# Kernel optimization log

Measured on AMD Instinct MI355X. Metric: run time of the kernel, lower is better.

The kernel has to match this reference:

```python
import jax, jax.numpy as jnp
import numpy as np

D = 256      # d_model
A = 64       # attn_dim
K = 16       # k_neighbors
N = 20000    # embedding table rows
B = 32768    # batch of perturbed genes
SCALE = A ** -0.5
EPS = 1e-5


def setup_inputs() -> dict:
    key = jax.random.key(0)
    ks = jax.random.split(key, 12)
    all_embs = jax.random.normal(ks[0], (N, D), dtype=jnp.float32)
    center_idx = jax.random.randint(ks[1], (B,), 0, N)
    nb_idx = jax.random.randint(ks[2], (B, K), 0, N)
    nb_weights = jax.random.uniform(ks[3], (B, K), dtype=jnp.float32)
    # learned params (torch Linear weight layout: [out, in])
    s = lambda fan_in: 1.0 / np.sqrt(fan_in)
    Wq = jax.random.uniform(ks[4], (A, D), minval=-s(D), maxval=s(D))
    Wk = jax.random.uniform(ks[5], (A, D), minval=-s(D), maxval=s(D))
    Wg = jax.random.uniform(ks[6], (D, D), minval=-s(D), maxval=s(D))
    bg = jax.random.uniform(ks[7], (D,), minval=-s(D), maxval=s(D))
    Wo = jax.random.uniform(ks[8], (D, 2 * D), minval=-s(2 * D), maxval=s(2 * D))
    bo = jax.random.uniform(ks[9], (D,), minval=-s(2 * D), maxval=s(2 * D))
    gamma = jnp.ones((D,), jnp.float32)
    beta = jnp.zeros((D,), jnp.float32)
    return dict(all_embs=all_embs, center_idx=center_idx, nb_idx=nb_idx,
                nb_weights=nb_weights, Wq=Wq, Wk=Wk, Wg=Wg, bg=bg,
                Wo=Wo, bo=bo, gamma=gamma, beta=beta)


def reference(all_embs, center_idx, nb_idx, nb_weights, Wq, Wk, Wg, bg, Wo, bo, gamma, beta):
    center = all_embs[center_idx]                      # [B, D]
    nbs = all_embs[nb_idx]                             # [B, K, D]
    q = center @ Wq.T                                  # [B, A]
    k = jnp.einsum('bkd,ad->bka', nbs, Wk)             # [B, K, A]
    logits = jnp.einsum('ba,bka->bk', q, k) * SCALE
    logits = logits + jnp.log(jnp.clip(nb_weights, 1e-6))
    attn = jax.nn.softmax(logits, axis=-1)             # [B, K]
    gate = jax.nn.sigmoid(center @ Wg.T + bg)          # [B, D]
    context = gate * jnp.einsum('bk,bkd->bd', attn, nbs)
    combined = jnp.concatenate([center, context], axis=-1)  # [B, 2D]
    enriched = combined @ Wo.T + bo                    # [B, D]
    x = enriched + center
    mu = jnp.mean(x, axis=-1, keepdims=True)
    var = jnp.var(x, axis=-1, keepdims=True)
    return (x - mu) * jax.lax.rsqrt(var + EPS) * gamma + beta
```

## Files before the change

kernel.cpp:

```cpp
#include <hip/hip_runtime.h>

#define DD 256
#define MM 16

typedef __attribute__((ext_vector_type(8))) short bfrag;
typedef __attribute__((ext_vector_type(4))) float ffrag;

__device__ __forceinline__ float lo2f(unsigned int p){ union{unsigned int i; float f;} v; v.i = p<<16; return v.f; }
__device__ __forceinline__ float hi2f(unsigned int p){ union{unsigned int i; float f;} v; v.i = p & 0xffff0000u; return v.f; }
__device__ __forceinline__ float bf2f(unsigned short u){ union{unsigned int i; float f;} v; v.i = ((unsigned int)u)<<16; return v.f; }
__device__ __forceinline__ unsigned short f2b(float x){
    union{float f; unsigned int i;} v; v.f = x;
    unsigned int r = v.i + 0x7fffu + ((v.i>>16)&1u);
    return (unsigned short)(r>>16);
}
__device__ __forceinline__ unsigned int pack2(float a, float b){
    return (unsigned int)f2b(a) | ((unsigned int)f2b(b)<<16);
}

__device__ __forceinline__ int swz256(int d, int e){
    return ((d>>4)*8 + (e>>5))*512 + (((e>>3)&3)*16 + (d&15))*8 + (e&7);
}
__device__ __forceinline__ int swz512(int d, int e){
    return ((d>>4)*16 + (e>>5))*512 + (((e>>3)&3)*16 + (d&15))*8 + (e&7);
}

extern "C" __global__ __launch_bounds__(256)
void prep_all(const float* __restrict__ Wq, const float* __restrict__ Wk,
              const float* __restrict__ Wg, const float* __restrict__ Wo,
              const float* __restrict__ embs, unsigned short* __restrict__ ws, int n8)
{
    int bid = blockIdx.x, e = threadIdx.x;
    if (bid < 256) {
        int d = bid; float acc = 0.f;
        #pragma unroll 8
        for (int a = 0; a < 64; ++a) acc = fmaf(Wq[a*256 + e], Wk[a*256 + d], acc);
        ws[swz256(d, e)] = f2b(acc);
    } else if (bid < 512) {
        int r = bid - 256;
        ws[65536 + swz256(r, e)] = f2b(Wg[r*256 + e]);
    } else if (bid < 768) {
        int r = bid - 512;
        ws[131072 + swz512(r, e)]       = f2b(Wo[r*512 + e]);
        ws[131072 + swz512(r, e + 256)] = f2b(Wo[r*512 + 256 + e]);
    } else {
        int i = (bid - 768)*256 + e;
        if (i < n8) {
            const float4* s = (const float4*)embs + (size_t)i*2;
            float4 a = s[0], b = s[1];
            uint4 o;
            o.x = pack2(a.x,a.y); o.y = pack2(a.z,a.w);
            o.z = pack2(b.x,b.y); o.w = pack2(b.z,b.w);
            ((uint4*)(ws + 262144))[i] = o;
        }
    }
}

template<bool TBF>
__device__ __forceinline__ void gather8(uint4* buf, const unsigned short* tbl,
                                        const float* embs, int idx, int p)
{
    if (TBF) {
        const unsigned short* base = tbl + (size_t)idx*DD + p*8;
        #pragma unroll
        for (int i = 0; i < 8; ++i) buf[i] = *(const uint4*)(base + i*32);
    } else {
        const float* base = embs + (size_t)idx*DD + p*8;
        #pragma unroll
        for (int i = 0; i < 8; ++i) {
            float4 a = *(const float4*)(base + i*32);
            float4 b = *(const float4*)(base + i*32 + 4);
            buf[i].x = pack2(a.x,a.y); buf[i].y = pack2(a.z,a.w);
            buf[i].z = pack2(b.x,b.y); buf[i].w = pack2(b.z,b.w);
        }
    }
}

template<bool TBF>
__global__ __launch_bounds__(256, 3)
void na_mfma6(const float* __restrict__ embs,
              const int* __restrict__ cidx,
              const int* __restrict__ nidx,
              const float* __restrict__ nbw,
              const unsigned short* __restrict__ tbl,
              const unsigned short* __restrict__ wMt,
              const unsigned short* __restrict__ wWg,
              const unsigned short* __restrict__ wWo,
              const float* __restrict__ bg,
              const float* __restrict__ bo,
              const float* __restrict__ gamma,
              const float* __restrict__ beta,
              float* __restrict__ out)
{
    __shared__ __align__(16) unsigned short s_ax[16][264];
    __shared__ __align__(16) unsigned short s_t[16][264];
    __shared__ __align__(16) unsigned short s_nb[4][16][264];
    __shared__ float s_attn[4][16];
    __shared__ int   s_cidx[16];
    float* s_x = (float*)&s_nb[0][0][0];

    const int tid  = threadIdx.x;
    const int row0 = blockIdx.x * MM;
    const int lane = tid & 63, wv = tid >> 6;
    const int l15  = lane & 15, quad = lane >> 4;
    const ffrag fz = {0.f, 0.f, 0.f, 0.f};

    if (tid < 16) s_cidx[tid] = cidx[row0 + tid];
    uint4 careg[8];
    {
        int aidx = cidx[row0 + l15];
        if (TBF) {
            const unsigned short* p = tbl + (size_t)aidx*DD + quad*8;
            #pragma unroll
            for (int kc = 0; kc < 8; ++kc) careg[kc] = *(const uint4*)(p + kc*32);
        } else {
            const float* p = embs + (size_t)aidx*DD + quad*8;
            #pragma unroll
            for (int kc = 0; kc < 8; ++kc) {
                float4 a = *(const float4*)(p + kc*32);
                float4 b = *(const float4*)(p + kc*32 + 4);
                careg[kc].x = pack2(a.x,a.y); careg[kc].y = pack2(a.z,a.w);
                careg[kc].z = pack2(b.x,b.y); careg[kc].w = pack2(b.z,b.w);
            }
        }
    }

    {
        ffrag at[4] = {fz,fz,fz,fz}, ag[4] = {fz,fz,fz,fz};
        const unsigned short* btA = wMt + (size_t)(wv*4)*4096 + lane*8;
        const unsigned short* bgA = wWg + (size_t)(wv*4)*4096 + lane*8;
        #pragma unroll
        for (int kc = 0; kc < 8; ++kc) {
            bfrag af = *(const bfrag*)&careg[kc];
            #pragma unroll
            for (int t = 0; t < 4; ++t) {
                at[t] = __builtin_amdgcn_mfma_f32_16x16x32_bf16(af, *(const bfrag*)(btA + t*4096 + kc*512), at[t], 0,0,0);
                ag[t] = __builtin_amdgcn_mfma_f32_16x16x32_bf16(af, *(const bfrag*)(bgA + t*4096 + kc*512), ag[t], 0,0,0);
            }
        }
        #pragma unroll
        for (int t = 0; t < 4; ++t) {
            int col = wv*64 + t*16 + l15;
            float bgv = bg[col];
            #pragma unroll
            for (int r = 0; r < 4; ++r) {
                int rr = quad*4 + r;
                s_t[rr][col]  = f2b(at[t][r]);
                float g = 1.f / (1.f + expf(-(ag[t][r] + bgv)));
                s_ax[rr][col] = f2b(g);
            }
        }
    }
    __syncthreads();

    {
        const int k = lane >> 2;
        const int p = lane & 3;
        int idxs[4];
        #pragma unroll
        for (int j = 0; j < 4; ++j)
            idxs[j] = nidx[(size_t)(row0 + 4*wv + j) * 16 + k];

        uint4 buf[2][8];
        gather8<TBF>(buf[0], tbl, embs, idxs[0], p);

        #pragma unroll
        for (int j = 0; j < 4; ++j) {
            if (j < 3) gather8<TBF>(buf[(j+1)&1], tbl, embs, idxs[j+1], p);
            const int m = 4*wv + j;
            unsigned short* nbp = &s_nb[wv][k][p*8];
            #pragma unroll
            for (int i = 0; i < 8; ++i) *(uint4*)(nbp + i*32) = buf[j&1][i];
            const unsigned short* trow = &s_t[m][p*8];
            float part = 0.f;
            #pragma unroll
            for (int i = 0; i < 8; ++i) {
                uint4 v = buf[j&1][i];
                uint4 tv = *(const uint4*)(trow + i*32);
                part += lo2f(v.x)*lo2f(tv.x) + hi2f(v.x)*hi2f(tv.x)
                      + lo2f(v.y)*lo2f(tv.y) + hi2f(v.y)*hi2f(tv.y)
                      + lo2f(v.z)*lo2f(tv.z) + hi2f(v.z)*hi2f(tv.z)
                      + lo2f(v.w)*lo2f(tv.w) + hi2f(v.w)*hi2f(tv.w);
            }
            part += __shfl_xor(part, 1);
            part += __shfl_xor(part, 2);
            float lg = part * 0.125f;
            float mx = lg;
            mx = fmaxf(mx, __shfl_xor(mx, 4));  mx = fmaxf(mx, __shfl_xor(mx, 8));
            mx = fmaxf(mx, __shfl_xor(mx, 16)); mx = fmaxf(mx, __shfl_xor(mx, 32));
            float wgt = fmaxf(nbw[(size_t)(row0 + m) * 16 + k], 1e-6f);
            float e = wgt * __expf(lg - mx);
            float s = e;
            s += __shfl_xor(s, 4);  s += __shfl_xor(s, 8);
            s += __shfl_xor(s, 16); s += __shfl_xor(s, 32);
            float attn = e / s;
            if (p == 0) s_attn[wv][k] = attn;
            float4 aw0 = *(const float4*)&s_attn[wv][0];
            float4 aw1 = *(const float4*)&s_attn[wv][4];
            float4 aw2 = *(const float4*)&s_attn[wv][8];
            float4 aw3 = *(const float4*)&s_attn[wv][12];
            float aarr[16] = {aw0.x,aw0.y,aw0.z,aw0.w, aw1.x,aw1.y,aw1.z,aw1.w,
                              aw2.x,aw2.y,aw2.z,aw2.w, aw3.x,aw3.y,aw3.z,aw3.w};
            float c0=0.f, c1=0.f, c2=0.f, c3=0.f;
            #pragma unroll
            for (int kk = 0; kk < 16; ++kk) {
                uint2 v = *(const uint2*)&s_nb[wv][kk][lane*4];
                float a = aarr[kk];
                c0 += a * lo2f(v.x); c1 += a * hi2f(v.x);
                c2 += a * lo2f(v.y); c3 += a * hi2f(v.y);
            }
            uint2 g = *(const uint2*)&s_ax[m][lane*4];
            c0 *= lo2f(g.x); c1 *= hi2f(g.x); c2 *= lo2f(g.y); c3 *= hi2f(g.y);
            uint2 o; o.x = pack2(c0, c1); o.y = pack2(c2, c3);
            *(uint2*)&s_ax[m][lane*4] = o;
        }
    }
    __syncthreads();

    {
        ffrag acc[4] = {fz,fz,fz,fz};
        const unsigned short* arx = &s_ax[l15][quad * 8];
        const unsigned short* bO  = wWo + (size_t)(wv*4)*8192 + lane*8;
        #pragma unroll
        for (int kc = 0; kc < 8; ++kc) {
            bfrag af = *(const bfrag*)&careg[kc];
            #pragma unroll
            for (int t = 0; t < 4; ++t)
                acc[t] = __builtin_amdgcn_mfma_f32_16x16x32_bf16(af, *(const bfrag*)(bO + t*8192 + kc*512), acc[t], 0,0,0);
        }
        #pragma unroll
        for (int kc = 8; kc < 16; ++kc) {
            bfrag af = *(const bfrag*)(arx + (kc-8)*32);
            #pragma unroll
            for (int t = 0; t < 4; ++t)
                acc[t] = __builtin_amdgcn_mfma_f32_16x16x32_bf16(af, *(const bfrag*)(bO + t*8192 + kc*512), acc[t], 0,0,0);
        }
        #pragma unroll
        for (int t = 0; t < 4; ++t) {
            int col = wv*64 + t*16 + l15;
            float bov = bo[col];
            #pragma unroll
            for (int r = 0; r < 4; ++r) {
                int rr = quad*4 + r;
                float ctr = embs[(size_t)s_cidx[rr] * DD + col];
                s_x[rr*260 + col] = acc[t][r] + bov + ctr;
            }
        }
    }
    __syncthreads();

    {
        #pragma unroll
        for (int jj = 0; jj < 4; ++jj) {
            int m = wv * 4 + jj;
            const float* xr = s_x + m*260;
            float x0 = xr[lane],       x1 = xr[64 + lane];
            float x2 = xr[128 + lane], x3 = xr[192 + lane];
            float s  = x0 + x1 + x2 + x3;
            float ss = x0*x0 + x1*x1 + x2*x2 + x3*x3;
            #pragma unroll
            for (int off = 32; off >= 1; off >>= 1) {
                s  += __shfl_xor(s, off);
                ss += __shfl_xor(ss, off);
            }
            float mu  = s * (1.f/256.f);
            float var = ss * (1.f/256.f) - mu*mu;
            float rs  = rsqrtf(var + 1e-5f);
            size_t base = (size_t)(row0 + m) * DD;
            float xs[4] = {x0, x1, x2, x3};
            #pragma unroll
            for (int cc = 0; cc < 4; ++cc) {
                int dd = cc*64 + lane;
                out[base + dd] = (xs[cc] - mu) * rs * gamma[dd] + beta[dd];
            }
        }
    }
}

#define SD 260
#define KT 16
#define WS 17
extern "C" __global__ __launch_bounds__(256)
void na_f32_kernel(const float* __restrict__ embs, const int* __restrict__ center_idx,
                   const int* __restrict__ nb_idx, const float* __restrict__ nb_w,
                   const float* __restrict__ Wq, const float* __restrict__ Wk,
                   const float* __restrict__ Wg, const float* __restrict__ bg,
                   const float* __restrict__ Wo, const float* __restrict__ bo,
                   const float* __restrict__ gamma, const float* __restrict__ beta,
                   float* __restrict__ out)
{
    __shared__ __align__(16) float s_center[MM][SD];
    __shared__ __align__(16) float s_tc[MM][SD];
    __shared__ __align__(16) float s_nb[16][SD];
    __shared__ __align__(16) float s_w[DD][WS];
    __shared__ __align__(16) float s_q[MM][64];
    __shared__ float s_red[16][16];
    __shared__ float s_attn[16];
    const int tid = threadIdx.x;
    const int row0 = blockIdx.x * MM;
    const int td = tid & 63, tm = tid >> 6;
    {
        int m = tid >> 4, c = tid & 15;
        int idx = center_idx[row0 + m];
        const float4* src = (const float4*)(embs + (size_t)idx * DD) + c * 4;
        float4* dst = (float4*)&s_center[m][c * 16];
        dst[0]=src[0]; dst[1]=src[1]; dst[2]=src[2]; dst[3]=src[3];
    }
    __syncthreads();
    {
        const int a = tid & 63, mg = tid >> 6;
        float qacc[4] = {0,0,0,0};
        for (int kt = 0; kt < DD; kt += KT) {
            __syncthreads();
            { int r = tid >> 2, c4 = (tid & 3) * 4;
              *(float4*)&s_w[r][c4] = *(const float4*)(Wq + r * DD + kt + c4); }
            __syncthreads();
            #pragma unroll
            for (int kk = 0; kk < KT; kk += 4) {
                float4 b = *(const float4*)&s_w[a][kk];
                #pragma unroll
                for (int i = 0; i < 4; ++i) {
                    float4 av = *(const float4*)&s_center[4*mg + i][kt + kk];
                    qacc[i] += av.x*b.x + av.y*b.y + av.z*b.z + av.w*b.w;
                }
            }
        }
        __syncthreads();
        #pragma unroll
        for (int i = 0; i < 4; ++i) s_q[4*mg + i][a] = qacc[i];
    }
    __syncthreads();
    {
        float tacc[4][4];
        #pragma unroll
        for (int i=0;i<4;++i) { tacc[i][0]=tacc[i][1]=tacc[i][2]=tacc[i][3]=0.f; }
        for (int kk = 0; kk < 64; kk += 4) {
            float4 bk[4];
            #pragma unroll
            for (int t4 = 0; t4 < 4; ++t4)
                bk[t4] = *(const float4*)(Wk + (size_t)(kk + t4) * DD + 4 * td);
            #pragma unroll
            for (int i = 0; i < 4; ++i) {
                float4 av = *(const float4*)&s_q[4*tm + i][kk];
                tacc[i][0] += av.x*bk[0].x + av.y*bk[1].x + av.z*bk[2].x + av.w*bk[3].x;
                tacc[i][1] += av.x*bk[0].y + av.y*bk[1].y + av.z*bk[2].y + av.w*bk[3].y;
                tacc[i][2] += av.x*bk[0].z + av.y*bk[1].z + av.z*bk[2].z + av.w*bk[3].z;
                tacc[i][3] += av.x*bk[0].w + av.y*bk[1].w + av.z*bk[2].w + av.w*bk[3].w;
            }
        }
        #pragma unroll
        for (int i = 0; i < 4; ++i)
            *(float4*)&s_tc[4*tm + i][4*td] = make_float4(tacc[i][0],tacc[i][1],tacc[i][2],tacc[i][3]);
    }
    __syncthreads();
    for (int m = 0; m < MM; ++m) {
        { int k = tid >> 4, c = tid & 15;
          int idx = nb_idx[(row0 + m) * 16 + k];
          const float4* src = (const float4*)(embs + (size_t)idx * DD) + c * 4;
          float4* dst = (float4*)&s_nb[k][c * 16];
          dst[0]=src[0]; dst[1]=src[1]; dst[2]=src[2]; dst[3]=src[3]; }
        __syncthreads();
        { int k = tid >> 4, i = tid & 15;
          float acc = 0.f;
          #pragma unroll
          for (int j4 = 0; j4 < 4; ++j4) {
              float4 nv = *(const float4*)&s_nb[k][i*16 + 4*j4];
              float4 tv = *(const float4*)&s_tc[m][i*16 + 4*j4];
              acc += nv.x*tv.x + nv.y*tv.y + nv.z*tv.z + nv.w*tv.w;
          }
          s_red[k][i] = acc; }
        __syncthreads();
        if (tid < 16) {
            float lg = 0.f;
            #pragma unroll
            for (int i = 0; i < 16; ++i) lg += s_red[tid][i];
            float wv2 = nb_w[(row0 + m) * 16 + tid];
            lg = lg * 0.125f + logf(fmaxf(wv2, 1e-6f));
            float mx = lg;
            #pragma unroll
            for (int off = 8; off >= 1; off >>= 1) mx = fmaxf(mx, __shfl_xor(mx, off));
            float e = expf(lg - mx);
            float s = e;
            #pragma unroll
            for (int off = 8; off >= 1; off >>= 1) s += __shfl_xor(s, off);
            s_attn[tid] = e / s;
        }
        __syncthreads();
        { float acc = 0.f;
// ... 93 lines not shown
            float mu = s * (1.f/256.f);
            float var = ss * (1.f/256.f) - mu*mu;
            float rs = rsqrtf(var + 1e-5f);
            size_t base = (size_t)(row0 + m) * DD;
            float xs[4] = {x0,x1,x2,x3};
            #pragma unroll
            for (int c = 0; c < 4; ++c) {
                int dd = c*64 + lane;
                out[base + dd] = (xs[c] - mu) * rs * gamma[dd] + beta[dd];
            }
        }
    }
}

extern "C" void kernel_launch(void* const* d_in, const int* in_sizes, int n_in,
                              void* d_out, int out_size, void* d_ws, size_t ws_size,
                              hipStream_t stream) {
    const float* embs  = (const float*)d_in[0];
    const int*   cidx  = (const int*)d_in[1];
    const int*   nidx  = (const int*)d_in[2];
    const float* nbw   = (const float*)d_in[3];
    const float* Wq    = (const float*)d_in[4];
    const float* Wk    = (const float*)d_in[5];
    const float* Wg    = (const float*)d_in[6];
    const float* bg    = (const float*)d_in[7];
    const float* Wo    = (const float*)d_in[8];
    const float* bo    = (const float*)d_in[9];
    const float* gamma = (const float*)d_in[10];
    const float* beta  = (const float*)d_in[11];
    float* out = (float*)d_out;

    const int B = in_sizes[1];
    const int nemb = in_sizes[0];
    const size_t need_w = 262144 * 2;
    const size_t need_t = need_w + (size_t)nemb * 2;

    if (ws_size < need_w) {
        hipLaunchKernelGGL(na_f32_kernel, dim3(B / MM), dim3(256), 0, stream,
                           embs, cidx, nidx, nbw, Wq, Wk, Wg, bg, Wo, bo, gamma, beta, out);
        return;
    }
    unsigned short* wsb = (unsigned short*)d_ws;
    const bool use_tbl = (ws_size >= need_t) && ((nemb & 7) == 0);
    const int n8 = use_tbl ? (nemb / 8) : 0;
    const int prep_grid = 768 + (use_tbl ? (n8 + 255) / 256 : 0);
    hipLaunchKernelGGL(prep_all, dim3(prep_grid), dim3(256), 0, stream,
                       Wq, Wk, Wg, Wo, embs, wsb, n8);

    if (use_tbl) {
        hipLaunchKernelGGL(na_mfma6<true>, dim3(B / MM), dim3(256), 0, stream,
                           embs, cidx, nidx, nbw, wsb + 262144,
                           wsb, wsb + 65536, wsb + 131072,
                           bg, bo, gamma, beta, out);
    } else {
        hipLaunchKernelGGL(na_mfma6<false>, dim3(B / MM), dim3(256), 0, stream,
                           embs, cidx, nidx, nbw, (const unsigned short*)nullptr,
                           wsb, wsb + 65536, wsb + 131072,
                           bg, bo, gamma, beta, out);
    }
}
```

Measured before the change: 175.6 us.

## Precompute key projection of embedding table and compute logits with MFMA

The prep kernel now projects the whole embedding table through Wk into a bf16 64-wide key table. It also stores Wq in bf16 instead of the fused 256x256 Wq^T·Wk matrix. The main kernel computes a 64-dim query per row and gets the 16 neighbor logits from two MFMAs over gathered key rows. This replaces the per-lane 256-element fp32 dot products and the wider query GEMM. The neighbor gather is also issued before the gate/query GEMM, center residual loads are hoisted ahead of the output GEMM, and the sigmoid uses __expf. The cost is extra prep work over the whole table and an additional 128-byte gather per neighbor.

```diff
diff --git a/kernel.cpp b/kernel.cpp
--- a/kernel.cpp
+++ b/kernel.cpp
@@ -25,33 +25,72 @@
     return ((d>>4)*16 + (e>>5))*512 + (((e>>3)&3)*16 + (d&15))*8 + (e&7);
 }
 
+#define OFF_WG 16384
+#define OFF_WO 81920
+#define OFF_KP 212992
+
 extern "C" __global__ __launch_bounds__(256)
 void prep_all(const float* __restrict__ Wq, const float* __restrict__ Wk,
               const float* __restrict__ Wg, const float* __restrict__ Wo,
-              const float* __restrict__ embs, unsigned short* __restrict__ ws, int n8)
+              const float* __restrict__ embs, unsigned short* __restrict__ ws,
+              int n8, int nrows, int nkpb)
 {
     int bid = blockIdx.x, e = threadIdx.x;
-    if (bid < 256) {
-        int d = bid; float acc = 0.f;
-        #pragma unroll 8
-        for (int a = 0; a < 64; ++a) acc = fmaf(Wq[a*256 + e], Wk[a*256 + d], acc);
-        ws[swz256(d, e)] = f2b(acc);
-    } else if (bid < 512) {
-        int r = bid - 256;
-        ws[65536 + swz256(r, e)] = f2b(Wg[r*256 + e]);
-    } else if (bid < 768) {
-        int r = bid - 512;
-        ws[131072 + swz512(r, e)]       = f2b(Wo[r*512 + e]);
-        ws[131072 + swz512(r, e + 256)] = f2b(Wo[r*512 + 256 + e]);
+    if (bid < 64) {
+        ws[swz256(bid, e)] = f2b(Wq[bid*256 + e]);
+    } else if (bid < 320) {
+        int r = bid - 64;
+        ws[OFF_WG + swz256(r, e)] = f2b(Wg[r*256 + e]);
+    } else if (bid < 576) {
+        int r = bid - 320;
+        ws[OFF_WO + swz512(r, e)]       = f2b(Wo[r*512 + e]);
+        ws[OFF_WO + swz512(r, e + 256)] = f2b(Wo[r*512 + 256 + e]);
+    } else if (bid < 576 + nkpb) {
+        int kb = bid - 576;
+        int wv = e >> 6, lane = e & 63, l15 = lane & 15, quad = lane >> 4;
+        int r0 = kb*64 + wv*16;
+        int arow = r0 + l15;
+        int arc  = arow < nrows ? arow : 0;
+        const float* ap = embs + (size_t)arc*256 + quad*8;
+        uint4 af[8];
+        #pragma unroll
+        for (int kc = 0; kc < 8; ++kc) {
+            float4 a = *(const float4*)(ap + kc*32);
+            float4 b = *(const float4*)(ap + kc*32 + 4);
+            af[kc].x = pack2(a.x,a.y); af[kc].y = pack2(a.z,a.w);
+            af[kc].z = pack2(b.x,b.y); af[kc].w = pack2(b.z,b.w);
+        }
+        const ffrag fz = {0.f,0.f,0.f,0.f};
+        #pragma unroll
+        for (int t = 0; t < 4; ++t) {
+            ffrag acc = fz;
+            const float* bp = Wk + (size_t)(t*16 + l15)*256 + quad*8;
+            #pragma unroll
+            for (int kc = 0; kc < 8; ++kc) {
+                float4 a = *(const float4*)(bp + kc*32);
+                float4 b = *(const float4*)(bp + kc*32 + 4);
+                uint4 bu;
+                bu.x = pack2(a.x,a.y); bu.y = pack2(a.z,a.w);
+                bu.z = pack2(b.x,b.y); bu.w = pack2(b.z,b.w);
+                acc = __builtin_amdgcn_mfma_f32_16x16x32_bf16(
+                        *(const bfrag*)&af[kc], *(const bfrag*)&bu, acc, 0,0,0);
+            }
+            #pragma unroll
+            for (int r = 0; r < 4; ++r) {
+                int orow = r0 + quad*4 + r;
+                if (orow < nrows)
+                    ws[OFF_KP + (size_t)orow*64 + t*16 + l15] = f2b(acc[r]);
+            }
+        }
     } else {
-        int i = (bid - 768)*256 + e;
+        int i = (bid - (576 + nkpb))*256 + e;
         if (i < n8) {
             const float4* s = (const float4*)embs + (size_t)i*2;
             float4 a = s[0], b = s[1];
             uint4 o;
             o.x = pack2(a.x,a.y); o.y = pack2(a.z,a.w);
             o.z = pack2(b.x,b.y); o.w = pack2(b.z,b.w);
-            ((uint4*)(ws + 262144))[i] = o;
+            ((uint4*)(ws + OFF_KP + (size_t)nrows*64))[i] = o;
         }
     }
 }
@@ -78,14 +117,15 @@
 
 template<bool TBF>
 __global__ __launch_bounds__(256, 3)
-void na_mfma6(const float* __restrict__ embs,
+void na_mfma7(const float* __restrict__ embs,
               const int* __restrict__ cidx,
               const int* __restrict__ nidx,
               const float* __restrict__ nbw,
               const unsigned short* __restrict__ tbl,
-              const unsigned short* __restrict__ wMt,
+              const unsigned short* __restrict__ wQ,
               const unsigned short* __restrict__ wWg,
               const unsigned short* __restrict__ wWo,
+              const unsigned short* __restrict__ kp,
               const float* __restrict__ bg,
               const float* __restrict__ bo,
               const float* __restrict__ gamma,
@@ -93,7 +133,7 @@
               float* __restrict__ out)
 {
     __shared__ __align__(16) unsigned short s_ax[16][264];
-    __shared__ __align__(16) unsigned short s_t[16][264];
+    __shared__ __align__(16) unsigned short s_q[16][72];
     __shared__ __align__(16) unsigned short s_nb[4][16][264];
     __shared__ float s_attn[4][16];
     __shared__ int   s_cidx[16];
@@ -110,34 +150,47 @@
     {
         int aidx = cidx[row0 + l15];
         if (TBF) {
-            const unsigned short* p = tbl + (size_t)aidx*DD + quad*8;
-            #pragma unroll
-            for (int kc = 0; kc < 8; ++kc) careg[kc] = *(const uint4*)(p + kc*32);
+            const unsigned short* pc = tbl + (size_t)aidx*DD + quad*8;
+            #pragma unroll
+            for (int kc = 0; kc < 8; ++kc) careg[kc] = *(const uint4*)(pc + kc*32);
         } else {
-            const float* p = embs + (size_t)aidx*DD + quad*8;
+            const float* pc = embs + (size_t)aidx*DD + quad*8;
             #pragma unroll
             for (int kc = 0; kc < 8; ++kc) {
-                float4 a = *(const float4*)(p + kc*32);
-                float4 b = *(const float4*)(p + kc*32 + 4);
+                float4 a = *(const float4*)(pc + kc*32);
+                float4 b = *(const float4*)(pc + kc*32 + 4);
                 careg[kc].x = pack2(a.x,a.y); careg[kc].y = pack2(a.z,a.w);
                 careg[kc].z = pack2(b.x,b.y); careg[kc].w = pack2(b.z,b.w);
             }
         }
     }
 
-    {
-        ffrag at[4] = {fz,fz,fz,fz}, ag[4] = {fz,fz,fz,fz};
-        const unsigned short* btA = wMt + (size_t)(wv*4)*4096 + lane*8;
+    const int kn = lane >> 2, p = lane & 3;
+    int idxs[4], lgi[4];
+    #pragma unroll
+    for (int j = 0; j < 4; ++j) {
+        idxs[j] = nidx[(size_t)(row0 + 4*wv + j) * 16 + kn];
+        lgi[j]  = nidx[(size_t)(row0 + 4*wv + j) * 16 + l15];
+    }
+    uint4 buf[2][8];
+    gather8<TBF>(buf[0], tbl, embs, idxs[0], p);
+
+    {
+        ffrag ag[4] = {fz,fz,fz,fz};
+        ffrag aq = fz;
         const unsigned short* bgA = wWg + (size_t)(wv*4)*4096 + lane*8;
+        const unsigned short* bqA = wQ  + (size_t)(wv*8)*512  + lane*8;
         #pragma unroll
         for (int kc = 0; kc < 8; ++kc) {
             bfrag af = *(const bfrag*)&careg[kc];
-            #pragma unroll
-            for (int t = 0; t < 4; ++t) {
-                at[t] = __builtin_amdgcn_mfma_f32_16x16x32_bf16(af, *(const bfrag*)(btA + t*4096 + kc*512), at[t], 0,0,0);
-                ag[t] = __builtin_amdgcn_mfma_f32_16x16x32_bf16(af, *(const bfrag*)(bgA + t*4096 + kc*512), ag[t], 0,0,0);
-            }
-        }
+            aq = __builtin_amdgcn_mfma_f32_16x16x32_bf16(af, *(const bfrag*)(bqA + kc*512), aq, 0,0,0);
+            #pragma unroll
+            for (int t = 0; t < 4; ++t)
+                ag[t] = __builtin_amdgcn_mfma_f32_16x16x32_bf16(af, *(const bfrag*)(bgA + (size_t)t*4096 + kc*512), ag[t], 0,0,0);
+        }
+        #pragma unroll
+        for (int r = 0; r < 4; ++r)
+            s_q[quad*4 + r][wv*16 + l15] = f2b(aq[r]);
         #pragma unroll
         for (int t = 0; t < 4; ++t) {
             int col = wv*64 + t*16 + l15;
@@ -145,8 +198,7 @@
             #pragma unroll
             for (int r = 0; r < 4; ++r) {
                 int rr = quad*4 + r;
-                s_t[rr][col]  = f2b(at[t][r]);
-                float g = 1.f / (1.f + expf(-(ag[t][r] + bgv)));
+                float g = 1.f / (1.f + __expf(-(ag[t][r] + bgv)));
                 s_ax[rr][col] = f2b(g);
             }
         }
@@ -154,47 +206,38 @@
     __syncthreads();
 
     {
-        const int k = lane >> 2;
-        const int p = lane & 3;
-        int idxs[4];
-        #pragma unroll
-        for (int j = 0; j < 4; ++j)
-            idxs[j] = nidx[(size_t)(row0 + 4*wv + j) * 16 + k];
-
-        uint4 buf[2][8];
-        gather8<TBF>(buf[0], tbl, embs, idxs[0], p);
-
         #pragma unroll
         for (int j = 0; j < 4; ++j) {
             if (j < 3) gather8<TBF>(buf[(j+1)&1], tbl, embs, idxs[j+1], p);
             const int m = 4*wv + j;
-            unsigned short* nbp = &s_nb[wv][k][p*8];
+            unsigned short* nbp = &s_nb[wv][kn][p*8];
             #pragma unroll
             for (int i = 0; i < 8; ++i) *(uint4*)(nbp + i*32) = buf[j&1][i];
-            const unsigned short* trow = &s_t[m][p*8];
-            float part = 0.f;
-            #pragma unroll
-            for (int i = 0; i < 8; ++i) {
-                uint4 v = buf[j&1][i];
-                uint4 tv = *(const uint4*)(trow + i*32);
-                part += lo2f(v.x)*lo2f(tv.x) + hi2f(v.x)*hi2f(tv.x)
-                      + lo2f(v.y)*lo2f(tv.y) + hi2f(v.y)*hi2f(tv.y)
-                      + lo2f(v.z)*lo2f(tv.z) + hi2f(v.z)*hi2f(tv.z)
-                      + lo2f(v.w)*lo2f(tv.w) + hi2f(v.w)*hi2f(tv.w);
-            }
-            part += __shfl_xor(part, 1);
-            part += __shfl_xor(part, 2);
-            float lg = part * 0.125f;
-            float mx = lg;
-            mx = fmaxf(mx, __shfl_xor(mx, 4));  mx = fmaxf(mx, __shfl_xor(mx, 8));
-            mx = fmaxf(mx, __shfl_xor(mx, 16)); mx = fmaxf(mx, __shfl_xor(mx, 32));
-            float wgt = fmaxf(nbw[(size_t)(row0 + m) * 16 + k], 1e-6f);
-            float e = wgt * __expf(lg - mx);
-            float s = e;
-            s += __shfl_xor(s, 4);  s += __shfl_xor(s, 8);
+
+            const unsigned short* kpr = kp + (size_t)lgi[j]*64 + quad*8;
+            bfrag a0 = *(const bfrag*)(kpr);
+            bfrag a1 = *(const bfrag*)(kpr + 32);
+            bfrag q0 = *(const bfrag*)&s_q[m][quad*8];
+            bfrag q1 = *(const bfrag*)&s_q[m][32 + quad*8];
+            ffrag lac = fz;
+            lac = __builtin_amdgcn_mfma_f32_16x16x32_bf16(a0, q0, lac, 0,0,0);
+            lac = __builtin_amdgcn_mfma_f32_16x16x32_bf16(a1, q1, lac, 0,0,0);
+            float4 w4 = *(const float4*)(nbw + (size_t)(row0 + m)*16 + quad*4);
+            float lg0 = lac[0]*0.125f, lg1 = lac[1]*0.125f;
+            float lg2 = lac[2]*0.125f, lg3 = lac[3]*0.125f;
+            float mx = fmaxf(fmaxf(lg0, lg1), fmaxf(lg2, lg3));
+            mx = fmaxf(mx, __shfl_xor(mx, 16));
+            mx = fmaxf(mx, __shfl_xor(mx, 32));
+            float e0 = fmaxf(w4.x, 1e-6f) * __expf(lg0 - mx);
+            float e1 = fmaxf(w4.y, 1e-6f) * __expf(lg1 - mx);
+            float e2 = fmaxf(w4.z, 1e-6f) * __expf(lg2 - mx);
+            float e3 = fmaxf(w4.w, 1e-6f) * __expf(lg3 - mx);
+            float s = e0 + e1 + e2 + e3;
             s += __shfl_xor(s, 16); s += __shfl_xor(s, 32);
-            float attn = e / s;
-            if (p == 0) s_attn[wv][k] = attn;
+            float inv = 1.f / s;
+            if (l15 == 0)
+                *(float4*)&s_attn[wv][quad*4] = make_float4(e0*inv, e1*inv, e2*inv, e3*inv);
+
             float4 aw0 = *(const float4*)&s_attn[wv][0];
             float4 aw1 = *(const float4*)&s_attn[wv][4];
             float4 aw2 = *(const float4*)&s_attn[wv][8];
@@ -218,6 +261,13 @@
     __syncthreads();
 
     {
+        float ctr[16];
+        #pragma unroll
+        for (int t = 0; t < 4; ++t)
+            #pragma unroll
+            for (int r = 0; r < 4; ++r)
+                ctr[t*4+r] = embs[(size_t)s_cidx[quad*4 + r] * DD + wv*64 + t*16 + l15];
+
         ffrag acc[4] = {fz,fz,fz,fz};
         const unsigned short* arx = &s_ax[l15][quad * 8];
         const unsigned short* bO  = wWo + (size_t)(wv*4)*8192 + lane*8;
@@ -226,14 +276,14 @@
             bfrag af = *(const bfrag*)&careg[kc];
             #pragma unroll
             for (int t = 0; t < 4; ++t)
-                acc[t] = __builtin_amdgcn_mfma_f32_16x16x32_bf16(af, *(const bfrag*)(bO + t*8192 + kc*512), acc[t], 0,0,0);
+                acc[t] = __builtin_amdgcn_mfma_f32_16x16x32_bf16(af, *(const bfrag*)(bO + (size_t)t*8192 + kc*512), acc[t], 0,0,0);
         }
         #pragma unroll
         for (int kc = 8; kc < 16; ++kc) {
             bfrag af = *(const bfrag*)(arx + (kc-8)*32);
             #pragma unroll
             for (int t = 0; t < 4; ++t)
-                acc[t] = __builtin_amdgcn_mfma_f32_16x16x32_bf16(af, *(const bfrag*)(bO + t*8192 + kc*512), acc[t], 0,0,0);
+                acc[t] = __builtin_amdgcn_mfma_f32_16x16x32_bf16(af, *(const bfrag*)(bO + (size_t)t*8192 + kc*512), acc[t], 0,0,0);
         }
         #pragma unroll
         for (int t = 0; t < 4; ++t) {
@@ -242,8 +292,7 @@
             #pragma unroll
             for (int r = 0; r < 4; ++r) {
                 int rr = quad*4 + r;
-                float ctr = embs[(size_t)s_cidx[rr] * DD + col];
-                s_x[rr*260 + col] = acc[t][r] + bov + ctr;
+                s_x[rr*260 + col] = acc[t][r] + bov + ctr[t*4+r];
             }
         }
     }
@@ -513,10 +562,13 @@
 
     const int B = in_sizes[1];
     const int nemb = in_sizes[0];
-    const size_t need_w = 262144 * 2;
+    const int nrows = nemb / 256;
+    const int nkpb = (nrows + 63) / 64;
+    const size_t kp_shorts = (size_t)nrows * 64;
+    const size_t need_w = ((size_t)OFF_KP + kp_shorts) * 2;
     const size_t need_t = need_w + (size_t)nemb * 2;
 
-    if (ws_size < need_w) {
+    if (ws_size < need_w || (nemb & 255) != 0) {
         hipLaunchKernelGGL(na_f32_kernel, dim3(B / MM), dim3(256), 0, stream,
                            embs, cidx, nidx, nbw, Wq, Wk, Wg, bg, Wo, bo, gamma, beta, out);
         return;
@@ -524,19 +576,21 @@
     unsigned short* wsb = (unsigned short*)d_ws;
     const bool use_tbl = (ws_size >= need_t) && ((nemb & 7) == 0);
     const int n8 = use_tbl ? (nemb / 8) : 0;
-    const int prep_grid = 768 + (use_tbl ? (n8 + 255) / 256 : 0);
+    const int prep_grid = 576 + nkpb + (use_tbl ? (n8 + 255) / 256 : 0);
     hipLaunchKernelGGL(prep_all, dim3(prep_grid), dim3(256), 0, stream,
-                       Wq, Wk, Wg, Wo, embs, wsb, n8);
-
+                       Wq, Wk, Wg, Wo, embs, wsb, n8, nrows, nkpb);
+
+    const unsigned short* kp  = wsb + OFF_KP;
+    const unsigned short* tbl = wsb + OFF_KP + kp_shorts;
     if (use_tbl) {
-        hipLaunchKernelGGL(na_mfma6<true>, dim3(B / MM), dim3(256), 0, stream,
-                           embs, cidx, nidx, nbw, wsb + 262144,
-                           wsb, wsb + 65536, wsb + 131072,
+        hipLaunchKernelGGL(na_mfma7<true>, dim3(B / MM), dim3(256), 0, stream,
+                           embs, cidx, nidx, nbw, tbl,
+                           wsb, wsb + OFF_WG, wsb + OFF_WO, kp,
                            bg, bo, gamma, beta, out);
     } else {
-        hipLaunchKernelGGL(na_mfma6<false>, dim3(B / MM), dim3(256), 0, stream,
+        hipLaunchKernelGGL(na_mfma7<false>, dim3(B / MM), dim3(256), 0, stream,
                            embs, cidx, nidx, nbw, (const unsigned short*)nullptr,
-                           wsb, wsb + 65536, wsb + 131072,
+                           wsb, wsb + OFF_WG, wsb + OFF_WO, kp,
                            bg, bo, gamma, beta, out);
     }
 }
```

Measured after the change: 250.9 us. 42.9% more time.

## Hoist neighbor gather before projection GEMM and compute logits with MFMA

Applied to the files above, without the earlier changes.

Moves the neighbor index load and the first neighbor-row gather ahead of the Q/gate MFMA phase, so gather latency overlaps the projection work. Replaces the per-lane scalar bf16 dot product for attention logits with a 16x16x32 MFMA over the LDS-staged neighbor tile, and simplifies the softmax to operate on four logits per lane. It also prefetches the center residual values into registers before the output GEMM and swaps expf for __expf in the gate sigmoid. The changes raise register pressure under a 3-waves launch bound and slightly change numerics.

```diff
diff --git a/kernel.cpp b/kernel.cpp
--- a/kernel.cpp
+++ b/kernel.cpp
@@ -78,7 +78,7 @@
 
 template<bool TBF>
 __global__ __launch_bounds__(256, 3)
-void na_mfma6(const float* __restrict__ embs,
+void na_mfma8(const float* __restrict__ embs,
               const int* __restrict__ cidx,
               const int* __restrict__ nidx,
               const float* __restrict__ nbw,
@@ -95,7 +95,7 @@
     __shared__ __align__(16) unsigned short s_ax[16][264];
     __shared__ __align__(16) unsigned short s_t[16][264];
     __shared__ __align__(16) unsigned short s_nb[4][16][264];
-    __shared__ float s_attn[4][16];
+    __shared__ __align__(16) float s_attn[4][16];
     __shared__ int   s_cidx[16];
     float* s_x = (float*)&s_nb[0][0][0];
 
@@ -110,20 +110,28 @@
     {
         int aidx = cidx[row0 + l15];
         if (TBF) {
-            const unsigned short* p = tbl + (size_t)aidx*DD + quad*8;
-            #pragma unroll
-            for (int kc = 0; kc < 8; ++kc) careg[kc] = *(const uint4*)(p + kc*32);
+            const unsigned short* pc = tbl + (size_t)aidx*DD + quad*8;
+            #pragma unroll
+            for (int kc = 0; kc < 8; ++kc) careg[kc] = *(const uint4*)(pc + kc*32);
         } else {
-            const float* p = embs + (size_t)aidx*DD + quad*8;
+            const float* pc = embs + (size_t)aidx*DD + quad*8;
             #pragma unroll
             for (int kc = 0; kc < 8; ++kc) {
-                float4 a = *(const float4*)(p + kc*32);
-                float4 b = *(const float4*)(p + kc*32 + 4);
+                float4 a = *(const float4*)(pc + kc*32);
+                float4 b = *(const float4*)(pc + kc*32 + 4);
                 careg[kc].x = pack2(a.x,a.y); careg[kc].y = pack2(a.z,a.w);
                 careg[kc].z = pack2(b.x,b.y); careg[kc].w = pack2(b.z,b.w);
             }
         }
     }
+
+    const int kn = lane >> 2, p = lane & 3;
+    int idxs[4];
+    #pragma unroll
+    for (int j = 0; j < 4; ++j)
+        idxs[j] = nidx[(size_t)(row0 + 4*wv + j) * 16 + kn];
+    uint4 buf[2][8];
+    gather8<TBF>(buf[0], tbl, embs, idxs[0], p);
 
     {
         ffrag at[4] = {fz,fz,fz,fz}, ag[4] = {fz,fz,fz,fz};
@@ -134,8 +142,8 @@
             bfrag af = *(const bfrag*)&careg[kc];
             #pragma unroll
             for (int t = 0; t < 4; ++t) {
-                at[t] = __builtin_amdgcn_mfma_f32_16x16x32_bf16(af, *(const bfrag*)(btA + t*4096 + kc*512), at[t], 0,0,0);
-                ag[t] = __builtin_amdgcn_mfma_f32_16x16x32_bf16(af, *(const bfrag*)(bgA + t*4096 + kc*512), ag[t], 0,0,0);
+                at[t] = __builtin_amdgcn_mfma_f32_16x16x32_bf16(af, *(const bfrag*)(btA + (size_t)t*4096 + kc*512), at[t], 0,0,0);
+                ag[t] = __builtin_amdgcn_mfma_f32_16x16x32_bf16(af, *(const bfrag*)(bgA + (size_t)t*4096 + kc*512), ag[t], 0,0,0);
             }
         }
         #pragma unroll
@@ -146,7 +154,7 @@
             for (int r = 0; r < 4; ++r) {
                 int rr = quad*4 + r;
                 s_t[rr][col]  = f2b(at[t][r]);
-                float g = 1.f / (1.f + expf(-(ag[t][r] + bgv)));
+                float g = 1.f / (1.f + __expf(-(ag[t][r] + bgv)));
                 s_ax[rr][col] = f2b(g);
             }
         }
@@ -154,47 +162,38 @@
     __syncthreads();
 
     {
-        const int k = lane >> 2;
-        const int p = lane & 3;
-        int idxs[4];
-        #pragma unroll
-        for (int j = 0; j < 4; ++j)
-            idxs[j] = nidx[(size_t)(row0 + 4*wv + j) * 16 + k];
-
-        uint4 buf[2][8];
-        gather8<TBF>(buf[0], tbl, embs, idxs[0], p);
-
         #pragma unroll
         for (int j = 0; j < 4; ++j) {
             if (j < 3) gather8<TBF>(buf[(j+1)&1], tbl, embs, idxs[j+1], p);
             const int m = 4*wv + j;
-            unsigned short* nbp = &s_nb[wv][k][p*8];
+            unsigned short* nbp = &s_nb[wv][kn][p*8];
             #pragma unroll
             for (int i = 0; i < 8; ++i) *(uint4*)(nbp + i*32) = buf[j&1][i];
-            const unsigned short* trow = &s_t[m][p*8];
-            float part = 0.f;
-            #pragma unroll
-            for (int i = 0; i < 8; ++i) {
-                uint4 v = buf[j&1][i];
-                uint4 tv = *(const uint4*)(trow + i*32);
-                part += lo2f(v.x)*lo2f(tv.x) + hi2f(v.x)*hi2f(tv.x)
-                      + lo2f(v.y)*lo2f(tv.y) + hi2f(v.y)*hi2f(tv.y)
-                      + lo2f(v.z)*lo2f(tv.z) + hi2f(v.z)*hi2f(tv.z)
-                      + lo2f(v.w)*lo2f(tv.w) + hi2f(v.w)*hi2f(tv.w);
-            }
-            part += __shfl_xor(part, 1);
-            part += __shfl_xor(part, 2);
-            float lg = part * 0.125f;
-            float mx = lg;
-            mx = fmaxf(mx, __shfl_xor(mx, 4));  mx = fmaxf(mx, __shfl_xor(mx, 8));
-            mx = fmaxf(mx, __shfl_xor(mx, 16)); mx = fmaxf(mx, __shfl_xor(mx, 32));
-            float wgt = fmaxf(nbw[(size_t)(row0 + m) * 16 + k], 1e-6f);
-            float e = wgt * __expf(lg - mx);
-            float s = e;
-            s += __shfl_xor(s, 4);  s += __shfl_xor(s, 8);
+
+            const unsigned short* anb  = &s_nb[wv][l15][quad*8];
+            const unsigned short* trow = &s_t[m][quad*8];
+            ffrag lac = fz;
+            #pragma unroll
+            for (int kc = 0; kc < 8; ++kc)
+                lac = __builtin_amdgcn_mfma_f32_16x16x32_bf16(
+                        *(const bfrag*)(anb + kc*32), *(const bfrag*)(trow + kc*32), lac, 0,0,0);
+
+            float4 w4 = *(const float4*)(nbw + (size_t)(row0 + m)*16 + quad*4);
+            float lg0 = lac[0]*0.125f, lg1 = lac[1]*0.125f;
+            float lg2 = lac[2]*0.125f, lg3 = lac[3]*0.125f;
+            float mx = fmaxf(fmaxf(lg0, lg1), fmaxf(lg2, lg3));
+            mx = fmaxf(mx, __shfl_xor(mx, 16));
+            mx = fmaxf(mx, __shfl_xor(mx, 32));
+            float e0 = fmaxf(w4.x, 1e-6f) * __expf(lg0 - mx);
+            float e1 = fmaxf(w4.y, 1e-6f) * __expf(lg1 - mx);
+            float e2 = fmaxf(w4.z, 1e-6f) * __expf(lg2 - mx);
+            float e3 = fmaxf(w4.w, 1e-6f) * __expf(lg3 - mx);
+            float s = e0 + e1 + e2 + e3;
             s += __shfl_xor(s, 16); s += __shfl_xor(s, 32);
-            float attn = e / s;
-            if (p == 0) s_attn[wv][k] = attn;
+            float inv = 1.f / s;
+            if (l15 == 0)
+                *(float4*)&s_attn[wv][quad*4] = make_float4(e0*inv, e1*inv, e2*inv, e3*inv);
+
             float4 aw0 = *(const float4*)&s_attn[wv][0];
             float4 aw1 = *(const float4*)&s_attn[wv][4];
             float4 aw2 = *(const float4*)&s_attn[wv][8];
@@ -218,6 +217,13 @@
     __syncthreads();
 
     {
+        float ctr[16];
+        #pragma unroll
+        for (int t = 0; t < 4; ++t)
+            #pragma unroll
+            for (int r = 0; r < 4; ++r)
+                ctr[t*4+r] = embs[(size_t)s_cidx[quad*4 + r] * DD + wv*64 + t*16 + l15];
+
         ffrag acc[4] = {fz,fz,fz,fz};
         const unsigned short* arx = &s_ax[l15][quad * 8];
         const unsigned short* bO  = wWo + (size_t)(wv*4)*8192 + lane*8;
@@ -226,14 +232,14 @@
             bfrag af = *(const bfrag*)&careg[kc];
             #pragma unroll
             for (int t = 0; t < 4; ++t)
-                acc[t] = __builtin_amdgcn_mfma_f32_16x16x32_bf16(af, *(const bfrag*)(bO + t*8192 + kc*512), acc[t], 0,0,0);
+                acc[t] = __builtin_amdgcn_mfma_f32_16x16x32_bf16(af, *(const bfrag*)(bO + (size_t)t*8192 + kc*512), acc[t], 0,0,0);
         }
         #pragma unroll
         for (int kc = 8; kc < 16; ++kc) {
             bfrag af = *(const bfrag*)(arx + (kc-8)*32);
             #pragma unroll
             for (int t = 0; t < 4; ++t)
-                acc[t] = __builtin_amdgcn_mfma_f32_16x16x32_bf16(af, *(const bfrag*)(bO + t*8192 + kc*512), acc[t], 0,0,0);
+                acc[t] = __builtin_amdgcn_mfma_f32_16x16x32_bf16(af, *(const bfrag*)(bO + (size_t)t*8192 + kc*512), acc[t], 0,0,0);
         }
         #pragma unroll
         for (int t = 0; t < 4; ++t) {
@@ -242,8 +248,7 @@
             #pragma unroll
             for (int r = 0; r < 4; ++r) {
                 int rr = quad*4 + r;
-                float ctr = embs[(size_t)s_cidx[rr] * DD + col];
-                s_x[rr*260 + col] = acc[t][r] + bov + ctr;
+                s_x[rr*260 + col] = acc[t][r] + bov + ctr[t*4+r];
             }
         }
     }
@@ -529,12 +534,12 @@
                        Wq, Wk, Wg, Wo, embs, wsb, n8);
 
     if (use_tbl) {
-        hipLaunchKernelGGL(na_mfma6<true>, dim3(B / MM), dim3(256), 0, stream,
+        hipLaunchKernelGGL(na_mfma8<true>, dim3(B / MM), dim3(256), 0, stream,
                            embs, cidx, nidx, nbw, wsb + 262144,
                            wsb, wsb + 65536, wsb + 131072,
                            bg, bo, gamma, beta, out);
     } else {
-        hipLaunchKernelGGL(na_mfma6<false>, dim3(B / MM), dim3(256), 0, stream,
+        hipLaunchKernelGGL(na_mfma8<false>, dim3(B / MM), dim3(256), 0, stream,
                            embs, cidx, nidx, nbw, (const unsigned short*)nullptr,
                            wsb, wsb + 65536, wsb + 131072,
                            bg, bo, gamma, beta, out);
```

Result: slower. 222.5 us (+26.7%).

## Process 32 rows per block, sharing weight fragments across two MFMA row tiles

Applied to the files above, without the earlier changes.

Doubles the rows per block from 16 to 32. Each B-fragment of the Wq·Wk, Wg and Wo weights loaded from global memory now feeds two MFMA row tiles, halving weight traffic per row. The neighbour attention phase runs twice per block and reuses an LDS arena for the t-vectors, neighbour buffers and the LayerNorm scratch. Attention weights are broadcast with wave shuffles instead of through LDS, and the sigmoid uses the fast exp. The cost is more registers and LDS per block (launch bounds drop to 2 blocks per CU) and half as many blocks, which may lower occupancy and latency hiding for the gathers.

```diff
diff --git a/kernel.cpp b/kernel.cpp
--- a/kernel.cpp
+++ b/kernel.cpp
@@ -1,7 +1,7 @@
 #include <hip/hip_runtime.h>
 
 #define DD 256
-#define MM 16
+#define MM 32
 
 typedef __attribute__((ext_vector_type(8))) short bfrag;
 typedef __attribute__((ext_vector_type(4))) float ffrag;
@@ -77,27 +77,28 @@
 }
 
 template<bool TBF>
-__global__ __launch_bounds__(256, 3)
-void na_mfma6(const float* __restrict__ embs,
-              const int* __restrict__ cidx,
-              const int* __restrict__ nidx,
-              const float* __restrict__ nbw,
-              const unsigned short* __restrict__ tbl,
-              const unsigned short* __restrict__ wMt,
-              const unsigned short* __restrict__ wWg,
-              const unsigned short* __restrict__ wWo,
-              const float* __restrict__ bg,
-              const float* __restrict__ bo,
-              const float* __restrict__ gamma,
-              const float* __restrict__ beta,
-              float* __restrict__ out)
+__global__ __launch_bounds__(256, 2)
+void na_mfma11(const float* __restrict__ embs,
+               const int* __restrict__ cidx,
+               const int* __restrict__ nidx,
+               const float* __restrict__ nbw,
+               const unsigned short* __restrict__ tbl,
+               const unsigned short* __restrict__ wMt,
+               const unsigned short* __restrict__ wWg,
+               const unsigned short* __restrict__ wWo,
+               const float* __restrict__ bg,
+               const float* __restrict__ bo,
+               const float* __restrict__ gamma,
+               const float* __restrict__ beta,
+               float* __restrict__ out)
 {
-    __shared__ __align__(16) unsigned short s_ax[16][264];
-    __shared__ __align__(16) unsigned short s_t[16][264];
-    __shared__ __align__(16) unsigned short s_nb[4][16][264];
-    __shared__ float s_attn[4][16];
-    __shared__ int   s_cidx[16];
-    float* s_x = (float*)&s_nb[0][0][0];
+    __shared__ __align__(16) unsigned short s_ax[32][264];
+    __shared__ __align__(16) unsigned short s_arena[21120];
+    __shared__ int s_cidx[32];
+
+    unsigned short (*s_t)[264]      = (unsigned short(*)[264])s_arena;
+    unsigned short (*s_nb)[16][264] = (unsigned short(*)[16][264])(s_arena + 4224);
+    float* s_x = (float*)s_arena;
 
     const int tid  = threadIdx.x;
     const int row0 = blockIdx.x * MM;
@@ -105,37 +106,54 @@
     const int l15  = lane & 15, quad = lane >> 4;
     const ffrag fz = {0.f, 0.f, 0.f, 0.f};
 
-    if (tid < 16) s_cidx[tid] = cidx[row0 + tid];
-    uint4 careg[8];
-    {
-        int aidx = cidx[row0 + l15];
+    if (tid < 32) s_cidx[tid] = cidx[row0 + tid];
+    uint4 careg0[8], careg1[8];
+    {
+        int a0 = cidx[row0 + l15];
+        int a1 = cidx[row0 + 16 + l15];
         if (TBF) {
-            const unsigned short* p = tbl + (size_t)aidx*DD + quad*8;
-            #pragma unroll
-            for (int kc = 0; kc < 8; ++kc) careg[kc] = *(const uint4*)(p + kc*32);
+            const unsigned short* p0 = tbl + (size_t)a0*DD + quad*8;
+            const unsigned short* p1 = tbl + (size_t)a1*DD + quad*8;
+            #pragma unroll
+            for (int kc = 0; kc < 8; ++kc) {
+                careg0[kc] = *(const uint4*)(p0 + kc*32);
+                careg1[kc] = *(const uint4*)(p1 + kc*32);
+            }
         } else {
-            const float* p = embs + (size_t)aidx*DD + quad*8;
+            const float* p0 = embs + (size_t)a0*DD + quad*8;
+            const float* p1 = embs + (size_t)a1*DD + quad*8;
             #pragma unroll
             for (int kc = 0; kc < 8; ++kc) {
-                float4 a = *(const float4*)(p + kc*32);
-                float4 b = *(const float4*)(p + kc*32 + 4);
-                careg[kc].x = pack2(a.x,a.y); careg[kc].y = pack2(a.z,a.w);
-                careg[kc].z = pack2(b.x,b.y); careg[kc].w = pack2(b.z,b.w);
-            }
-        }
-    }
-
-    {
-        ffrag at[4] = {fz,fz,fz,fz}, ag[4] = {fz,fz,fz,fz};
+                float4 a = *(const float4*)(p0 + kc*32);
+                float4 b = *(const float4*)(p0 + kc*32 + 4);
+                careg0[kc].x = pack2(a.x,a.y); careg0[kc].y = pack2(a.z,a.w);
+                careg0[kc].z = pack2(b.x,b.y); careg0[kc].w = pack2(b.z,b.w);
+                float4 c = *(const float4*)(p1 + kc*32);
+                float4 d = *(const float4*)(p1 + kc*32 + 4);
+                careg1[kc].x = pack2(c.x,c.y); careg1[kc].y = pack2(c.z,c.w);
+                careg1[kc].z = pack2(d.x,d.y); careg1[kc].w = pack2(d.z,d.w);
+            }
+        }
+    }
+
+    ffrag at1[4] = {fz,fz,fz,fz};
+    {
+        ffrag at0[4] = {fz,fz,fz,fz};
+        ffrag ag0[4] = {fz,fz,fz,fz}, ag1[4] = {fz,fz,fz,fz};
         const unsigned short* btA = wMt + (size_t)(wv*4)*4096 + lane*8;
         const unsigned short* bgA = wWg + (size_t)(wv*4)*4096 + lane*8;
         #pragma unroll
         for (int kc = 0; kc < 8; ++kc) {
-            bfrag af = *(const bfrag*)&careg[kc];
+            bfrag a0 = *(const bfrag*)&careg0[kc];
+            bfrag a1 = *(const bfrag*)&careg1[kc];
             #pragma unroll
             for (int t = 0; t < 4; ++t) {
-                at[t] = __builtin_amdgcn_mfma_f32_16x16x32_bf16(af, *(const bfrag*)(btA + t*4096 + kc*512), at[t], 0,0,0);
-                ag[t] = __builtin_amdgcn_mfma_f32_16x16x32_bf16(af, *(const bfrag*)(bgA + t*4096 + kc*512), ag[t], 0,0,0);
+                bfrag bm = *(const bfrag*)(btA + (size_t)t*4096 + kc*512);
+                at0[t] = __builtin_amdgcn_mfma_f32_16x16x32_bf16(a0, bm, at0[t], 0,0,0);
+                at1[t] = __builtin_amdgcn_mfma_f32_16x16x32_bf16(a1, bm, at1[t], 0,0,0);
+                bfrag bw = *(const bfrag*)(bgA + (size_t)t*4096 + kc*512);
+                ag0[t] = __builtin_amdgcn_mfma_f32_16x16x32_bf16(a0, bw, ag0[t], 0,0,0);
+                ag1[t] = __builtin_amdgcn_mfma_f32_16x16x32_bf16(a1, bw, ag1[t], 0,0,0);
             }
         }
         #pragma unroll
@@ -145,21 +163,23 @@
             #pragma unroll
             for (int r = 0; r < 4; ++r) {
                 int rr = quad*4 + r;
-                s_t[rr][col]  = f2b(at[t][r]);
-                float g = 1.f / (1.f + expf(-(ag[t][r] + bgv)));
-                s_ax[rr][col] = f2b(g);
-            }
-        }
-    }
-    __syncthreads();
-
-    {
-        const int k = lane >> 2;
-        const int p = lane & 3;
+                s_t[rr][col] = f2b(at0[t][r]);
+                float g0 = 1.f / (1.f + __expf(-(ag0[t][r] + bgv)));
+                s_ax[rr][col] = f2b(g0);
+                float g1 = 1.f / (1.f + __expf(-(ag1[t][r] + bgv)));
+                s_ax[16 + rr][col] = f2b(g1);
+            }
+        }
+    }
+    __syncthreads();
+
+    const int kn = lane >> 2;
+    const int p  = lane & 3;
+    auto attn_phase = [&](int rb) {
         int idxs[4];
         #pragma unroll
         for (int j = 0; j < 4; ++j)
-            idxs[j] = nidx[(size_t)(row0 + 4*wv + j) * 16 + k];
+            idxs[j] = nidx[(size_t)(row0 + rb + 4*wv + j) * 16 + kn];
 
         uint4 buf[2][8];
         gather8<TBF>(buf[0], tbl, embs, idxs[0], p);
@@ -167,11 +187,12 @@
         #pragma unroll
         for (int j = 0; j < 4; ++j) {
             if (j < 3) gather8<TBF>(buf[(j+1)&1], tbl, embs, idxs[j+1], p);
-            const int m = 4*wv + j;
-            unsigned short* nbp = &s_nb[wv][k][p*8];
+            const int ml = 4*wv + j;
+            const int mg = rb + ml;
+            unsigned short* nbp = &s_nb[wv][kn][p*8];
             #pragma unroll
             for (int i = 0; i < 8; ++i) *(uint4*)(nbp + i*32) = buf[j&1][i];
-            const unsigned short* trow = &s_t[m][p*8];
+            const unsigned short* trow = &s_t[ml][p*8];
             float part = 0.f;
             #pragma unroll
             for (int i = 0; i < 8; ++i) {
@@ -188,52 +209,68 @@
             float mx = lg;
             mx = fmaxf(mx, __shfl_xor(mx, 4));  mx = fmaxf(mx, __shfl_xor(mx, 8));
             mx = fmaxf(mx, __shfl_xor(mx, 16)); mx = fmaxf(mx, __shfl_xor(mx, 32));
-            float wgt = fmaxf(nbw[(size_t)(row0 + m) * 16 + k], 1e-6f);
+            float wgt = fmaxf(nbw[(size_t)(row0 + mg) * 16 + kn], 1e-6f);
             float e = wgt * __expf(lg - mx);
             float s = e;
             s += __shfl_xor(s, 4);  s += __shfl_xor(s, 8);
             s += __shfl_xor(s, 16); s += __shfl_xor(s, 32);
             float attn = e / s;
-            if (p == 0) s_attn[wv][k] = attn;
-            float4 aw0 = *(const float4*)&s_attn[wv][0];
-            float4 aw1 = *(const float4*)&s_attn[wv][4];
-            float4 aw2 = *(const float4*)&s_attn[wv][8];
-            float4 aw3 = *(const float4*)&s_attn[wv][12];
-            float aarr[16] = {aw0.x,aw0.y,aw0.z,aw0.w, aw1.x,aw1.y,aw1.z,aw1.w,
-                              aw2.x,aw2.y,aw2.z,aw2.w, aw3.x,aw3.y,aw3.z,aw3.w};
             float c0=0.f, c1=0.f, c2=0.f, c3=0.f;
             #pragma unroll
             for (int kk = 0; kk < 16; ++kk) {
+                float a = __shfl(attn, kk*4);
                 uint2 v = *(const uint2*)&s_nb[wv][kk][lane*4];
-                float a = aarr[kk];
                 c0 += a * lo2f(v.x); c1 += a * hi2f(v.x);
                 c2 += a * lo2f(v.y); c3 += a * hi2f(v.y);
             }
-            uint2 g = *(const uint2*)&s_ax[m][lane*4];
+            uint2 g = *(const uint2*)&s_ax[mg][lane*4];
             c0 *= lo2f(g.x); c1 *= hi2f(g.x); c2 *= lo2f(g.y); c3 *= hi2f(g.y);
             uint2 o; o.x = pack2(c0, c1); o.y = pack2(c2, c3);
-            *(uint2*)&s_ax[m][lane*4] = o;
-        }
-    }
-    __syncthreads();
-
-    {
-        ffrag acc[4] = {fz,fz,fz,fz};
-        const unsigned short* arx = &s_ax[l15][quad * 8];
-        const unsigned short* bO  = wWo + (size_t)(wv*4)*8192 + lane*8;
+            *(uint2*)&s_ax[mg][lane*4] = o;
+        }
+    };
+
+    attn_phase(0);
+    __syncthreads();
+    {
+        #pragma unroll
+        for (int t = 0; t < 4; ++t) {
+            int col = wv*64 + t*16 + l15;
+            #pragma unroll
+            for (int r = 0; r < 4; ++r)
+                s_t[quad*4 + r][col] = f2b(at1[t][r]);
+        }
+    }
+    __syncthreads();
+    attn_phase(16);
+    __syncthreads();
+
+    {
+        ffrag acc0[4] = {fz,fz,fz,fz}, acc1[4] = {fz,fz,fz,fz};
+        const unsigned short* arx0 = &s_ax[l15][quad * 8];
+        const unsigned short* arx1 = &s_ax[16 + l15][quad * 8];
+        const unsigned short* bO   = wWo + (size_t)(wv*4)*8192 + lane*8;
         #pragma unroll
         for (int kc = 0; kc < 8; ++kc) {
-            bfrag af = *(const bfrag*)&careg[kc];
-            #pragma unroll
-            for (int t = 0; t < 4; ++t)
-                acc[t] = __builtin_amdgcn_mfma_f32_16x16x32_bf16(af, *(const bfrag*)(bO + t*8192 + kc*512), acc[t], 0,0,0);
+            bfrag a0 = *(const bfrag*)&careg0[kc];
+            bfrag a1 = *(const bfrag*)&careg1[kc];
+            #pragma unroll
+            for (int t = 0; t < 4; ++t) {
+                bfrag b = *(const bfrag*)(bO + (size_t)t*8192 + kc*512);
+                acc0[t] = __builtin_amdgcn_mfma_f32_16x16x32_bf16(a0, b, acc0[t], 0,0,0);
+                acc1[t] = __builtin_amdgcn_mfma_f32_16x16x32_bf16(a1, b, acc1[t], 0,0,0);
+            }
         }
         #pragma unroll
         for (int kc = 8; kc < 16; ++kc) {
-            bfrag af = *(const bfrag*)(arx + (kc-8)*32);
-            #pragma unroll
-            for (int t = 0; t < 4; ++t)
-                acc[t] = __builtin_amdgcn_mfma_f32_16x16x32_bf16(af, *(const bfrag*)(bO + t*8192 + kc*512), acc[t], 0,0,0);
+            bfrag a0 = *(const bfrag*)(arx0 + (kc-8)*32);
+            bfrag a1 = *(const bfrag*)(arx1 + (kc-8)*32);
+            #pragma unroll
+            for (int t = 0; t < 4; ++t) {
+                bfrag b = *(const bfrag*)(bO + (size_t)t*8192 + kc*512);
+                acc0[t] = __builtin_amdgcn_mfma_f32_16x16x32_bf16(a0, b, acc0[t], 0,0,0);
+                acc1[t] = __builtin_amdgcn_mfma_f32_16x16x32_bf16(a1, b, acc1[t], 0,0,0);
+            }
         }
         #pragma unroll
         for (int t = 0; t < 4; ++t) {
@@ -242,17 +279,19 @@
             #pragma unroll
             for (int r = 0; r < 4; ++r) {
                 int rr = quad*4 + r;
-                float ctr = embs[(size_t)s_cidx[rr] * DD + col];
-                s_x[rr*260 + col] = acc[t][r] + bov + ctr;
-            }
-        }
-    }
-    __syncthreads();
-
-    {
-        #pragma unroll
-        for (int jj = 0; jj < 4; ++jj) {
-            int m = wv * 4 + jj;
+                float c0 = embs[(size_t)s_cidx[rr] * DD + col];
+                s_x[rr*260 + col] = acc0[t][r] + bov + c0;
+                float c1 = embs[(size_t)s_cidx[16 + rr] * DD + col];
+                s_x[(16 + rr)*260 + col] = acc1[t][r] + bov + c1;
+            }
+        }
+    }
+    __syncthreads();
+
+    {
+        #pragma unroll
+        for (int jj = 0; jj < 8; ++jj) {
+            int m = wv * 8 + jj;
             const float* xr = s_x + m*260;
             float x0 = xr[lane],       x1 = xr[64 + lane];
             float x2 = xr[128 + lane], x3 = xr[192 + lane];
@@ -280,6 +319,7 @@
 #define SD 260
 #define KT 16
 #define WS 17
+#define FM 16
 extern "C" __global__ __launch_bounds__(256)
 void na_f32_kernel(const float* __restrict__ embs, const int* __restrict__ center_idx,
                    const int* __restrict__ nb_idx, const float* __restrict__ nb_w,
@@ -289,15 +329,15 @@
                    const float* __restrict__ gamma, const float* __restrict__ beta,
                    float* __restrict__ out)
 {
-    __shared__ __align__(16) float s_center[MM][SD];
-    __shared__ __align__(16) float s_tc[MM][SD];
+    __shared__ __align__(16) float s_center[FM][SD];
+    __shared__ __align__(16) float s_tc[FM][SD];
     __shared__ __align__(16) float s_nb[16][SD];
     __shared__ __align__(16) float s_w[DD][WS];
-    __shared__ __align__(16) float s_q[MM][64];
+    __shared__ __align__(16) float s_q[FM][64];
     __shared__ float s_red[16][16];
     __shared__ float s_attn[16];
     const int tid = threadIdx.x;
-    const int row0 = blockIdx.x * MM;
+    const int row0 = blockIdx.x * FM;
     const int td = tid & 63, tm = tid >> 6;
     {
         int m = tid >> 4, c = tid & 15;
@@ -353,7 +393,7 @@
             *(float4*)&s_tc[4*tm + i][4*td] = make_float4(tacc[i][0],tacc[i][1],tacc[i][2],tacc[i][3]);
     }
     __syncthreads();
-    for (int m = 0; m < MM; ++m) {
+    for (int m = 0; m < FM; ++m) {
         { int k = tid >> 4, c = tid & 15;
           int idx = nb_idx[(row0 + m) * 16 + k];
           const float4* src = (const float4*)(embs + (size_t)idx * DD) + c * 4;
@@ -516,8 +556,8 @@
     const size_t need_w = 262144 * 2;
     const size_t need_t = need_w + (size_t)nemb * 2;
 
-    if (ws_size < need_w) {
-        hipLaunchKernelGGL(na_f32_kernel, dim3(B / MM), dim3(256), 0, stream,
+    if (ws_size < need_w || (B & 31) != 0) {
+        hipLaunchKernelGGL(na_f32_kernel, dim3(B / FM), dim3(256), 0, stream,
                            embs, cidx, nidx, nbw, Wq, Wk, Wg, bg, Wo, bo, gamma, beta, out);
         return;
     }
@@ -529,12 +569,12 @@
                        Wq, Wk, Wg, Wo, embs, wsb, n8);
 
     if (use_tbl) {
-        hipLaunchKernelGGL(na_mfma6<true>, dim3(B / MM), dim3(256), 0, stream,
+        hipLaunchKernelGGL(na_mfma11<true>, dim3(B / MM), dim3(256), 0, stream,
                            embs, cidx, nidx, nbw, wsb + 262144,
                            wsb, wsb + 65536, wsb + 131072,
                            bg, bo, gamma, beta, out);
     } else {
-        hipLaunchKernelGGL(na_mfma6<false>, dim3(B / MM), dim3(256), 0, stream,
+        hipLaunchKernelGGL(na_mfma11<false>, dim3(B / MM), dim3(256), 0, stream,
                            embs, cidx, nidx, nbw, (const unsigned short*)nullptr,
                            wsb, wsb + 65536, wsb + 131072,
                            bg, bo, gamma, beta, out);
```

Measured after the change: 172.8 us. No clear change (-1.6%).
